# Kernel optimization log

Hardware: AMD Instinct MI355X
Metric: run time of the kernel (lower is better)

Reference implementation:

```python
import jax, jax.numpy as jnp
import numpy as np

# Block(type='a'): dim=256, mlp_ratio=2, qk_dim=64, att_cr=0.5 (pdim=128), sr=2, inp_group=1
DIM, QK, PD, HID, SR = 256, 64, 128, 512, 2
EPS = 1e-5
SCALE = QK ** -0.5


def _conv(x, w, stride=1, pad=0, groups=1):
    return jax.lax.conv_general_dilated(
        x, w, (stride, stride), [(pad, pad), (pad, pad)],
        feature_group_count=groups,
        dimension_numbers=('NCHW', 'OIHW', 'NCHW'))


def _bn(x, s, b):
    # BatchNorm2d in inference/reparam form: per-channel affine
    return x * s[:, None, None] + b[:, None, None]


def setup_inputs() -> dict:
    key = jax.random.key(0)
    ks = jax.random.split(key, 16)
    B, H, W = 16, 64, 64
    x = jax.random.normal(ks[0], (B, DIM, H, W), jnp.float32)
    def w(k, shape):  # conv weights
        return jax.random.normal(k, shape, jnp.float32) * 0.02
    def sb(k, c):     # bn scale / bias
        k1, k2 = jax.random.split(k)
        return (1.0 + 0.1 * jax.random.normal(k1, (c,), jnp.float32),
                0.1 * jax.random.normal(k2, (c,), jnp.float32))
    s_in, b_in = sb(ks[2], 2 * QK + DIM)
    s_k, b_k = sb(ks[4], QK)
    s_v, b_v = sb(ks[6], PD)
    s_out, b_out = sb(ks[8], DIM)
    s1, b1 = sb(ks[10], HID)
    s2, b2 = sb(ks[12], DIM)
    return dict(
        x=x,
        gn_w=1.0 + 0.1 * jax.random.normal(ks[13], (DIM,), jnp.float32),
        gn_b=0.1 * jax.random.normal(ks[14], (DIM,), jnp.float32),
        w_in=w(ks[1], (2 * QK + DIM, DIM, 3, 3)), s_in=s_in, b_in=b_in,
        w_k=w(ks[3], (QK, 1, SR, SR)), s_k=s_k, b_k=b_k,
        w_v=w(ks[5], (PD, 1, SR, SR)), s_v=s_v, b_v=b_v,
        w_out=w(ks[7], (DIM, DIM, 1, 1)), s_out=s_out, b_out=b_out,
        w1=w(ks[9], (HID, DIM, 1, 1)), s1=s1, b1=b1,
        w2=w(ks[11], (DIM, HID, 1, 1)), s2=s2, b2=b2,
    )


def reference(x, gn_w, gn_b, w_in, s_in, b_in, w_k, s_k, b_k, w_v, s_v, b_v,
              w_out, s_out, b_out, w1, s1, b1, w2, s2, b2):
    B, _, H, W = x.shape
    # --- LRSHA branch ---
    # GroupNorm(1, dim): normalize over (C,H,W) per sample, per-channel affine
    mu = jnp.mean(x, axis=(1, 2, 3), keepdims=True)
    var = jnp.var(x, axis=(1, 2, 3), keepdims=True)
    xn = (x - mu) * jax.lax.rsqrt(var + EPS)
    xn = xn * gn_w[:, None, None] + gn_b[:, None, None]
    t = _bn(_conv(xn, w_in, stride=1, pad=1), s_in, b_in)  # [B, 2*QK+DIM, H, W]
    q, k, v, u = jnp.split(t, [QK, 2 * QK, 2 * QK + PD], axis=1)
    k = _bn(_conv(k, w_k, stride=SR, groups=QK), s_k, b_k)  # [B,QK,H/2,W/2]
    v = _bn(_conv(v, w_v, stride=SR, groups=PD), s_v, b_v)  # [B,PD,H/2,W/2]
    qf = q.reshape(B, QK, H * W)          # [B, QK, N]
    kf = k.reshape(B, QK, -1)             # [B, QK, M]
    vf = v.reshape(B, PD, -1)             # [B, PD, M]
    attn = jax.nn.softmax(jnp.einsum('bcn,bcm->bnm', qf, kf) * SCALE, axis=-1)
    a = jnp.einsum('bpm,bnm->bpn', vf, attn).reshape(B, PD, H, W)
    cat = jnp.concatenate([a, u], axis=1)  # [B, DIM, H, W]
    att_out = _bn(_conv(jax.nn.relu(cat), w_out), s_out, b_out)
    x1 = x + att_out  # residual
    # --- FFN branch (1x1 conv -> ReLU -> 1x1 conv) ---
    h = jax.nn.relu(_bn(_conv(x1, w1), s1, b1))
    ffn = _bn(_conv(h, w2), s2, b2)
    return x1 + ffn
```

## Files before the change

kernel.cpp:

```cpp
#include <hip/hip_runtime.h>
#include <hip/hip_bf16.h>

#define DIM 256
#define QK 64
#define PD 128
#define HID 512
#define NPX 4096
#define NB 16
#define SCALE 0.125f
#define GN_EPS 1e-5f

typedef short bf16x8 __attribute__((ext_vector_type(8)));
typedef float f32x4 __attribute__((ext_vector_type(4)));
#define MFMA16(a, b, c) __builtin_amdgcn_mfma_f32_16x16x32_bf16(a, b, c, 0, 0, 0)

__device__ __forceinline__ unsigned f2b(float f) {
    unsigned u = __float_as_uint(f);
    return (u + 0x7fffu + ((u >> 16) & 1u)) >> 16;
}
__device__ __forceinline__ float b2f(unsigned short s) {
    return __uint_as_float((unsigned)s << 16);
}

__global__ __launch_bounds__(256) void gn_part_kernel(const float* __restrict__ x, float* __restrict__ part) {
    int chunk = blockIdx.x, b = blockIdx.y;
    const float* xp = x + (size_t)b * (DIM * NPX) + (size_t)chunk * 16384;
    float s = 0.f, ss = 0.f;
    for (int i = threadIdx.x; i < 16384; i += 256) { float v = xp[i]; s += v; ss += v * v; }
    for (int off = 32; off > 0; off >>= 1) { s += __shfl_down(s, off); ss += __shfl_down(ss, off); }
    __shared__ float red[8];
    int w = threadIdx.x >> 6;
    if ((threadIdx.x & 63) == 0) { red[w * 2] = s; red[w * 2 + 1] = ss; }
    __syncthreads();
    if (threadIdx.x == 0) {
        float S = red[0] + red[2] + red[4] + red[6];
        float SS = red[1] + red[3] + red[5] + red[7];
        part[(b * 64 + chunk) * 2] = S;
        part[(b * 64 + chunk) * 2 + 1] = SS;
    }
}

__global__ __launch_bounds__(256) void gn_final_kernel(const float* __restrict__ part,
                                                       const float* __restrict__ gn_w, const float* __restrict__ gn_b,
                                                       float* __restrict__ Aarr, float* __restrict__ Barr) {
    int b = blockIdx.x;
    float s = 0.f, ss = 0.f;
    if (threadIdx.x < 64) {
        s = part[(b * 64 + threadIdx.x) * 2];
        ss = part[(b * 64 + threadIdx.x) * 2 + 1];
        for (int off = 32; off > 0; off >>= 1) { s += __shfl_down(s, off); ss += __shfl_down(ss, off); }
    }
    __shared__ float sh[2];
    if (threadIdx.x == 0) {
        const float invN = 1.f / (float)(DIM * NPX);
        float mu = s * invN;
        float var = ss * invN - mu * mu;
        sh[0] = mu; sh[1] = rsqrtf(var + GN_EPS);
    }
    __syncthreads();
    float mu = sh[0], rstd = sh[1];
    int c = threadIdx.x;
    float g = gn_w[c] * rstd;
    Aarr[b * 256 + c] = g;
    Barr[b * 256 + c] = gn_b[c] - mu * g;
}

__global__ __launch_bounds__(256) void xnb_kernel(const float* __restrict__ x,
                                                  const float* __restrict__ Aarr, const float* __restrict__ Barr,
                                                  unsigned short* __restrict__ xb) {
    int y = blockIdx.x, b = blockIdx.y;
    int tid = threadIdx.x;
    __shared__ unsigned short tile[64 * 264];
    const float* xr = x + ((size_t)b << 20) + (size_t)y * 64;
    const float* Ab = Aarr + b * 256;
    const float* Bb = Barr + b * 256;
    for (int it = 0; it < 64; it++) {
        int lin = it * 256 + tid;
        int c = lin >> 6, px = lin & 63;
        float v = fmaf(xr[((size_t)c << 12) + px], Ab[c], Bb[c]);
        tile[px * 264 + c] = (unsigned short)f2b(v);
    }
    __syncthreads();
    unsigned short* ob = xb + (((size_t)(b * 64 + y)) << 14);
    for (int it = 0; it < 8; it++) {
        int lin = it * 256 + tid;
        int px = lin >> 5, g = lin & 31;
        *(uint4*)&ob[px * 256 + g * 8] = *(const uint4*)&tile[px * 264 + g * 8];
    }
}

__global__ __launch_bounds__(256) void wcvt_kernel(const float* __restrict__ w_in, const float* __restrict__ w_out,
                                                   const float* __restrict__ w1, const float* __restrict__ w2,
                                                   unsigned short* __restrict__ wb2, unsigned short* __restrict__ wob,
                                                   unsigned short* __restrict__ w1b, unsigned short* __restrict__ w2b) {
    int idx = blockIdx.x * 256 + threadIdx.x;
    if (idx < 884736) {
        int ci = idx & 31;
        int oc = (idx >> 5) % 384;
        int tapck = idx / 12288;
        int ck = tapck / 9, tap = tapck % 9;
        wb2[idx] = (unsigned short)f2b(w_in[((size_t)oc * 256 + ck * 32 + ci) * 9 + tap]);
    } else if (idx < 950272) {
        int j = idx - 884736;
        wob[j] = (unsigned short)f2b(w_out[j]);
    } else if (idx < 1081344) {
        int j = idx - 950272;
        w1b[j] = (unsigned short)f2b(w1[j]);
    } else if (idx < 1212416) {
        int j = idx - 1081344;
        w2b[j] = (unsigned short)f2b(w2[j]);
    }
}

__global__ __launch_bounds__(256, 3) void conv3_mfma_kernel(const unsigned short* __restrict__ xb,
                                                            const unsigned short* __restrict__ wb2,
                                                            const float* __restrict__ s_in, const float* __restrict__ b_in,
                                                            unsigned short* __restrict__ tcl) {
    int wgid = blockIdx.x;
    int tile = (wgid & 7) * 96 + (wgid >> 3);
    int ocb = tile % 6;
    int tmp = tile / 6;
    int rg2 = tmp & 7, b = tmp >> 3;
    int tid = threadIdx.x;
    int w = tid >> 6, lane = tid & 63, g = lane >> 4, l15 = lane & 15;
    __shared__ unsigned short xs[6 * 66 * 40];
    int oc0 = ocb * 64;
    if (tid < 48) {
        int row = tid >> 3, cp = (tid >> 2) & 1, gg = tid & 3;
        int col = cp ? 65 : 0;
        *(uint4*)&xs[(row * 66 + col) * 40 + gg * 8] = make_uint4(0, 0, 0, 0);
    }
    const unsigned short* xg = xb + ((size_t)b << 20);
    for (int half = 0; half < 2; half++) {
        int y0 = rg2 * 8 + half * 4;
        f32x4 acc[4][4];
#pragma unroll
        for (int o = 0; o < 4; o++)
#pragma unroll
            for (int p = 0; p < 4; p++)
#pragma unroll
                for (int r = 0; r < 4; r++) acc[o][p][r] = 0.f;
        for (int ck = 0; ck < 8; ck++) {
            int ci0 = ck * 32;
            __syncthreads();
#pragma unroll
            for (int it = 0; it < 6; it++) {
                int lin = it * 256 + tid;
                int gg = lin & 3, col = (lin >> 2) & 63, row = lin >> 8;
                int y = y0 - 1 + row;
                uint4 val = make_uint4(0, 0, 0, 0);
                if (y >= 0 && y < 64)
                    val = *(const uint4*)(xg + (((size_t)(y * 64 + col)) << 8) + ci0 + gg * 8);
                *(uint4*)&xs[(row * 66 + col + 1) * 40 + gg * 8] = val;
            }
            __syncthreads();
            const unsigned short* wp = wb2 + (size_t)ck * 9 * 384 * 32;
#pragma unroll
            for (int tap = 0; tap < 9; tap++) {
                int dy = tap / 3, dx = tap % 3;
                bf16x8 Af[4], Bf[4];
#pragma unroll
                for (int o = 0; o < 4; o++)
                    Af[o] = *(const bf16x8*)(wp + ((size_t)tap * 384 + oc0 + o * 16 + l15) * 32 + g * 8);
#pragma unroll
                for (int p = 0; p < 4; p++)
                    Bf[p] = *(const bf16x8*)&xs[((w + dy) * 66 + p * 16 + l15 + dx) * 40 + g * 8];
#pragma unroll
                for (int o = 0; o < 4; o++)
#pragma unroll
                    for (int p = 0; p < 4; p++)
                        acc[o][p] = MFMA16(Af[o], Bf[p], acc[o][p]);
            }
        }
        int y = y0 + w;
        unsigned short* tout = tcl + ((size_t)(b * 4096 + y * 64)) * 384;
#pragma unroll
        for (int o = 0; o < 4; o++) {
            int ocb4 = oc0 + o * 16 + 4 * g;
            float s0 = s_in[ocb4], s1 = s_in[ocb4 + 1], s2 = s_in[ocb4 + 2], s3 = s_in[ocb4 + 3];
            float b0 = b_in[ocb4], b1 = b_in[ocb4 + 1], b2 = b_in[ocb4 + 2], b3 = b_in[ocb4 + 3];
#pragma unroll
            for (int p = 0; p < 4; p++) {
                ushort4 h;
                h.x = (unsigned short)f2b(fmaf(acc[o][p][0], s0, b0));
                h.y = (unsigned short)f2b(fmaf(acc[o][p][1], s1, b1));
                h.z = (unsigned short)f2b(fmaf(acc[o][p][2], s2, b2));
                h.w = (unsigned short)f2b(fmaf(acc[o][p][3], s3, b3));
                *(ushort4*)&tout[(size_t)(p * 16 + l15) * 384 + ocb4] = h;
            }
        }
    }
}

__global__ __launch_bounds__(256) void dw_kernel(const unsigned short* __restrict__ tcl,
                                                 const float* __restrict__ w_k, const float* __restrict__ s_k, const float* __restrict__ b_k,
                                                 const float* __restrict__ w_v, const float* __restrict__ s_v, const float* __restrict__ b_v,
                                                 unsigned short* __restrict__ kd_t, unsigned short* __restrict__ vd_b) {
    int mg = blockIdx.x, b = blockIdx.y;
    int m0 = mg * 64;
    int tid = threadIdx.x;
    __shared__ unsigned short vt[128 * 68];
    {
        int c = tid & 63;
        float4 wk4 = *(const float4*)(w_k + c * 4);
        float sc = s_k[c], bi = b_k[c];
#pragma unroll 4
        for (int it = 0; it < 16; it++) {
            int ml = it * 4 + (tid >> 6);
            int m = m0 + ml, yo = m >> 5, xo = m & 31;
            const unsigned short* s = tcl + ((size_t)(b * 4096 + yo * 128 + xo * 2)) * 384 + 64 + c;
            float v = wk4.x * b2f(s[0]) + wk4.y * b2f(s[384]) + wk4.z * b2f(s[24576]) + wk4.w * b2f(s[24960]);
            kd_t[((size_t)(b * 1024 + m) << 6) + c] = (unsigned short)f2b(fmaf(v, sc, bi));
        }
    }
    {
        int c2 = tid & 127;
        float4 wv4 = *(const float4*)(w_v + c2 * 4);
        float sc = s_v[c2], bi = b_v[c2];
#pragma unroll 4
        for (int it = 0; it < 32; it++) {
            int ml = it * 2 + (tid >> 7);
            int m = m0 + ml, yo = m >> 5, xo = m & 31;
            const unsigned short* s = tcl + ((size_t)(b * 4096 + yo * 128 + xo * 2)) * 384 + 128 + c2;
            float v = wv4.x * b2f(s[0]) + wv4.y * b2f(s[384]) + wv4.z * b2f(s[24576]) + wv4.w * b2f(s[24960]);
            vt[c2 * 68 + ml] = (unsigned short)f2b(fmaf(v, sc, bi));
        }
    }
    __syncthreads();
    {
        int c2 = tid >> 1, part = tid & 1;
        unsigned short* dst = vd_b + (((size_t)(b * 128 + c2)) << 10) + m0 + part * 32;
        const unsigned short* src = &vt[c2 * 68 + part * 32];
#pragma unroll
        for (int j = 0; j < 8; j++)
            *(ushort4*)(dst + j * 4) = *(const ushort4*)(src + j * 4);
    }
}

__global__ __launch_bounds__(256) void attn_mfma_kernel(const unsigned short* __restrict__ tcl,
                                                        const unsigned short* __restrict__ kd_t,
                                                        const unsigned short* __restrict__ vd_b,
                                                        float* __restrict__ a_out) {
    int tid = threadIdx.x;
    int wid = tid >> 6, lane = tid & 63;
    int g = lane >> 4, l15 = lane & 15;
    int b = blockIdx.y;
    int n0 = (blockIdx.x * 4 + wid) * 32;

    __shared__ char KsB[8192];
    __shared__ char VsB[16384];

    bf16x8 qf[2][2];
#pragma unroll
    for (int nf = 0; nf < 2; nf++)
#pragma unroll
        for (int kc = 0; kc < 2; kc++)
            qf[nf][kc] = *(const bf16x8*)(tcl + ((size_t)(b * 4096 + n0 + 16 * nf + l15)) * 384 + kc * 32 + g * 8);

    f32x4 O[8][2];
#pragma unroll
    for (int pt = 0; pt < 8; pt++)
#pragma unroll
        for (int nf = 0; nf < 2; nf++)
#pragma unroll
            for (int r = 0; r < 4; r++) O[pt][nf][r] = 0.f;
    float mr[2] = {-1e30f, -1e30f}, lr[2] = {0.f, 0.f};

    const unsigned short* kb = kd_t + ((size_t)b << 16);
    const unsigned short* vb = vd_b + ((size_t)(b * 128) << 10);

    union BU { unsigned u[4]; bf16x8 v; };
    int srcA = l15 + ((g & 1) << 5);
    int srcB = srcA + 16;
    bool hi = (g >> 1) != 0;
    int srow = tid >> 3, sch = tid & 7;

    for (int mt = 0; mt < 16; mt++) {
        int m0 = mt * 64;
        __syncthreads();
#pragma unroll
        for (int it = 0; it < 2; it++) {
            int row = it * 32 + srow;
            uint4 v = *(const uint4*)(kb + (((size_t)(m0 + row)) << 6) + sch * 8);
            *(uint4*)(KsB + row * 128 + ((sch * 16) ^ ((row & 7) << 4))) = v;
        }
#pragma unroll
        for (int it = 0; it < 4; it++) {
            int row = it * 32 + srow;
            uint4 v = *(const uint4*)(vb + (((size_t)row) << 10) + m0 + sch * 8);
            *(uint4*)(VsB + row * 128 + ((sch * 16) ^ ((row & 7) << 4))) = v;
        }
        __syncthreads();
        f32x4 sp[4][2];
#pragma unroll
        for (int f = 0; f < 4; f++)
#pragma unroll
            for (int nf = 0; nf < 2; nf++)
#pragma unroll
                for (int r = 0; r < 4; r++) sp[f][nf][r] = 0.f;
#pragma unroll
        for (int f = 0; f < 4; f++) {
#pragma unroll
            for (int kc = 0; kc < 2; kc++) {
                bf16x8 kf = *(const bf16x8*)(KsB + (16 * f + l15) * 128 + ((kc * 64 + g * 16) ^ ((l15 & 7) << 4)));
                sp[f][0] = MFMA16(kf, qf[0][kc], sp[f][0]);
                sp[f][1] = MFMA16(kf, qf[1][kc], sp[f][1]);
            }
        }
        BU Bp[2][2];
#pragma unroll
        for (int nf = 0; nf < 2; nf++) {
            float tmax = -1e30f;
#pragma unroll
            for (int f = 0; f < 4; f++)
#pragma unroll
                for (int r = 0; r < 4; r++) tmax = fmaxf(tmax, sp[f][nf][r]);
            tmax = fmaxf(tmax, __shfl_xor(tmax, 16));
            tmax = fmaxf(tmax, __shfl_xor(tmax, 32));
            float newm = fmaxf(mr[nf], tmax * SCALE);
            float fac = __expf(mr[nf] - newm);
            float ps = 0.f;
            unsigned pl[4], ph[4];
#pragma unroll
            for (int f = 0; f < 4; f++) {
                float p0 = __expf(fmaf(sp[f][nf][0], SCALE, -newm));
                float p1 = __expf(fmaf(sp[f][nf][1], SCALE, -newm));
                float p2 = __expf(fmaf(sp[f][nf][2], SCALE, -newm));
                float p3 = __expf(fmaf(sp[f][nf][3], SCALE, -newm));
                ps += (p0 + p1) + (p2 + p3);
                pl[f] = f2b(p0) | (f2b(p1) << 16);
                ph[f] = f2b(p2) | (f2b(p3) << 16);
            }
            ps += __shfl_xor(ps, 16);
            ps += __shfl_xor(ps, 32);
            lr[nf] = fmaf(lr[nf], fac, ps);
            mr[nf] = newm;
#pragma unroll
            for (int pt = 0; pt < 8; pt++)
#pragma unroll
                for (int r = 0; r < 4; r++) O[pt][nf][r] *= fac;
#pragma unroll
            for (int kc = 0; kc < 2; kc++) {
                unsigned a0 = (unsigned)__shfl((int)pl[2 * kc], srcA);
                unsigned a1 = (unsigned)__shfl((int)ph[2 * kc], srcA);
                unsigned b0 = (unsigned)__shfl((int)pl[2 * kc + 1], srcA);
                unsigned b1 = (unsigned)__shfl((int)ph[2 * kc + 1], srcA);
                unsigned a2 = (unsigned)__shfl((int)pl[2 * kc], srcB);
                unsigned a3 = (unsigned)__shfl((int)ph[2 * kc], srcB);
                unsigned b2 = (unsigned)__shfl((int)pl[2 * kc + 1], srcB);
                unsigned b3 = (unsigned)__shfl((int)ph[2 * kc + 1], srcB);
                Bp[nf][kc].u[0] = hi ? b0 : a0;
                Bp[nf][kc].u[1] = hi ? b1 : a1;
                Bp[nf][kc].u[2] = hi ? b2 : a2;
                Bp[nf][kc].u[3] = hi ? b3 : a3;
            }
        }
#pragma unroll
        for (int pt = 0; pt < 8; pt++) {
            int p = pt * 16 + l15;
#pragma unroll
            for (int kc = 0; kc < 2; kc++) {
                bf16x8 vf = *(const bf16x8*)(VsB + p * 128 + ((kc * 64 + g * 16) ^ ((p & 7) << 4)));
                O[pt][0] = MFMA16(vf, Bp[0][kc].v, O[pt][0]);
                O[pt][1] = MFMA16(vf, Bp[1][kc].v, O[pt][1]);
            }
        }
    }
    float inv0 = 1.f / lr[0], inv1 = 1.f / lr[1];
#pragma unroll
    for (int pt = 0; pt < 8; pt++) {
#pragma unroll
        for (int r = 0; r < 4; r++) {
            int prow = pt * 16 + 4 * g + r;
            size_t base = (((size_t)(b * 128 + prow)) << 12) + n0 + l15;
            a_out[base] = O[pt][0][r] * inv0;
            a_out[base + 16] = O[pt][1][r] * inv1;
        }
    }
}

__global__ __launch_bounds__(256) void acl_kernel(const float* __restrict__ a_in, const unsigned short* __restrict__ tcl,
                                                  unsigned short* __restrict__ aucl) {
    int ng = blockIdx.x, b = blockIdx.y;
    int tid = threadIdx.x;
    __shared__ unsigned short tile[64 * 132];
    int n0 = ng * 64;
    int nl = tid & 63, c4 = tid >> 6;
    for (int it = 0; it < 32; it++) {
        int ci = it * 4 + c4;
        float v = a_in[(((size_t)b * 128 + ci) << 12) + n0 + nl];
        tile[nl * 132 + ci] = (unsigned short)f2b(fmaxf(v, 0.f));
    }
    __syncthreads();
    for (int it = 0; it < 4; it++) {
        int lin = it * 256 + tid;
        int n = lin >> 4, cg = lin & 15;
        *(uint4*)&aucl[((size_t)(b * 4096 + n0 + n)) * 256 + cg * 8] = *(const uint4*)&tile[n * 132 + cg * 8];
    }
    for (int it = 0; it < 4; it++) {
        int lin = it * 256 + tid;
        int n = lin >> 4, cg = lin & 15;
        bf16x8 v = *(const bf16x8*)(tcl + ((size_t)(b * 4096 + n0 + n)) * 384 + 256 + cg * 8);
#pragma unroll
        for (int j = 0; j < 8; j++) {
            unsigned short s = (unsigned short)v[j];
            v[j] = (short)((s & 0x8000u) ? 0 : s);
        }
        *(bf16x8*)(aucl + ((size_t)(b * 4096 + n0 + n)) * 256 + 128 + cg * 8) = v;
    }
}

__global__ __launch_bounds__(256) void catconv_mfma_kernel(const unsigned short* __restrict__ aucl,
                                                           const unsigned short* __restrict__ wob,
                                                           const float* __restrict__ x,
                                                           const float* __restrict__ s_out, const float* __restrict__ b_out,
                                                           float* __restrict__ out, unsigned short* __restrict__ x1cl) {
    int tid = threadIdx.x;
    int w = tid >> 6, lane = tid & 63, g = lane >> 4, l15 = lane & 15;
    int b = blockIdx.z;
    int px0 = blockIdx.x * 256 + w * 64;
    int co0 = blockIdx.y * 64;
    f32x4 acc[4][4];
#pragma unroll
    for (int o = 0; o < 4; o++)
#pragma unroll
        for (int p = 0; p < 4; p++)
#pragma unroll
            for (int r = 0; r < 4; r++) acc[o][p][r] = 0.f;
    const unsigned short* ab = aucl + (((size_t)b * 4096) << 8);
    for (int kc = 0; kc < 8; kc++) {
        bf16x8 Af[4], Bf[4];
#pragma unroll
        for (int o = 0; o < 4; o++)
            Af[o] = *(const bf16x8*)(wob + (size_t)(co0 + o * 16 + l15) * 256 + kc * 32 + g * 8);
#pragma unroll
        for (int p = 0; p < 4; p++)
            Bf[p] = *(const bf16x8*)(ab + ((size_t)(px0 + p * 16 + l15) << 8) + kc * 32 + g * 8);
#pragma unroll
        for (int o = 0; o < 4; o++)
#pragma unroll
            for (int p = 0; p < 4; p++)
                acc[o][p] = MFMA16(Af[o], Bf[p], acc[o][p]);
    }
#pragma unroll
    for (int o = 0; o < 4; o++) {
        int co_b = co0 + o * 16 + 4 * g;
#pragma unroll
        for (int r = 0; r < 4; r++) {
            int co = co_b + r;
            float sc = s_out[co], bi = b_out[co];
            size_t base = (((size_t)b * 256 + co) << 12) + px0 + l15;
#pragma unroll
            for (int p = 0; p < 4; p++) {
                float res = x[base + p * 16] + fmaf(acc[o][p][r], sc, bi);
                out[base + p * 16] = res;
                acc[o][p][r] = res;
            }
        }
#pragma unroll
        for (int p = 0; p < 4; p++) {
            ushort4 h;
            h.x = (unsigned short)f2b(acc[o][p][0]);
            h.y = (unsigned short)f2b(acc[o][p][1]);
            h.z = (unsigned short)f2b(acc[o][p][2]);
            h.w = (unsigned short)f2b(acc[o][p][3]);
            *(ushort4*)&x1cl[((size_t)(b * 4096 + px0 + p * 16 + l15)) * 256 + co_b] = h;
        }
    }
}

__global__ __launch_bounds__(256) void ffn1_mfma_kernel(const unsigned short* __restrict__ x1cl,
                                                        const unsigned short* __restrict__ w1b,
                                                        const float* __restrict__ s1, const float* __restrict__ b1,
                                                        unsigned short* __restrict__ hcl) {
    int tid = threadIdx.x;
    int w = tid >> 6, lane = tid & 63, g = lane >> 4, l15 = lane & 15;
    int b = blockIdx.z;
    int px0 = blockIdx.x * 256 + w * 64;
    int hc0 = blockIdx.y * 64;
    f32x4 acc[4][4];
#pragma unroll
    for (int p = 0; p < 4; p++)
#pragma unroll
        for (int o = 0; o < 4; o++)
#pragma unroll
            for (int r = 0; r < 4; r++) acc[p][o][r] = 0.f;
    const unsigned short* xb = x1cl + (((size_t)b * 4096) << 8);
    for (int kc = 0; kc < 8; kc++) {
        bf16x8 Af[4], Bf[4];
#pragma unroll
        for (int p = 0; p < 4; p++)
            Af[p] = *(const bf16x8*)(xb + ((size_t)(px0 + p * 16 + l15) << 8) + kc * 32 + g * 8);
#pragma unroll
        for (int o = 0; o < 4; o++)
            Bf[o] = *(const bf16x8*)(w1b + (size_t)(hc0 + o * 16 + l15) * 256 + kc * 32 + g * 8);
#pragma unroll
        for (int p = 0; p < 4; p++)
#pragma unroll
            for (int o = 0; o < 4; o++)
                acc[p][o] = MFMA16(Af[p], Bf[o], acc[p][o]);
    }
    unsigned short* hb = hcl + (((size_t)b * 4096) << 9);
#pragma unroll
    for (int o = 0; o < 4; o++) {
        int hc = hc0 + o * 16 + l15;
        float sc = s1[hc], bi = b1[hc];
#pragma unroll
        for (int p = 0; p < 4; p++) {
#pragma unroll
            for (int r = 0; r < 4; r++) {
                int px = px0 + p * 16 + 4 * g + r;
                hb[((size_t)px << 9) + hc] = (unsigned short)f2b(fmaxf(fmaf(acc[p][o][r], sc, bi), 0.f));
            }
        }
    }
}

__global__ __launch_bounds__(256) void ffn2_mfma_kernel(const unsigned short* __restrict__ hcl,
                                                        const unsigned short* __restrict__ w2b,
                                                        const float* __restrict__ s2, const float* __restrict__ b2,
                                                        float* __restrict__ out) {
    int tid = threadIdx.x;
    int w = tid >> 6, lane = tid & 63, g = lane >> 4, l15 = lane & 15;
    int b = blockIdx.z;
    int px0 = blockIdx.x * 256 + w * 64;
    int co0 = blockIdx.y * 64;
    f32x4 acc[4][4];
#pragma unroll
    for (int o = 0; o < 4; o++)
#pragma unroll
        for (int p = 0; p < 4; p++)
#pragma unroll
            for (int r = 0; r < 4; r++) acc[o][p][r] = 0.f;
    const unsigned short* hb = hcl + (((size_t)b * 4096) << 9);
    for (int kc = 0; kc < 16; kc++) {
        bf16x8 Af[4], Bf[4];
#pragma unroll
        for (int o = 0; o < 4; o++)
            Af[o] = *(const bf16x8*)(w2b + (size_t)(co0 + o * 16 + l15) * 512 + kc * 32 + g * 8);
#pragma unroll
        for (int p = 0; p < 4; p++)
            Bf[p] = *(const bf16x8*)(hb + ((size_t)(px0 + p * 16 + l15) << 9) + kc * 32 + g * 8);
#pragma unroll
        for (int o = 0; o < 4; o++)
#pragma unroll
            for (int p = 0; p < 4; p++)
                acc[o][p] = MFMA16(Af[o], Bf[p], acc[o][p]);
    }
#pragma unroll
    for (int o = 0; o < 4; o++) {
#pragma unroll
        for (int r = 0; r < 4; r++) {
            int co = co0 + o * 16 + 4 * g + r;
            float sc = s2[co], bi = b2[co];
            size_t base = (((size_t)b * 256 + co) << 12) + px0 + l15;
#pragma unroll
            for (int p = 0; p < 4; p++)
                out[base + p * 16] = out[base + p * 16] + fmaf(acc[o][p][r], sc, bi);
        }
    }
}

extern "C" void kernel_launch(void* const* d_in, const int* in_sizes, int n_in,
                              void* d_out, int out_size, void* d_ws, size_t ws_size,
                              hipStream_t stream) {
    const float* x    = (const float*)d_in[0];
    const float* gn_w = (const float*)d_in[1];
    const float* gn_b = (const float*)d_in[2];
    const float* w_in = (const float*)d_in[3];
    const float* s_in = (const float*)d_in[4];
    const float* b_in = (const float*)d_in[5];
    const float* w_k  = (const float*)d_in[6];
    const float* s_k  = (const float*)d_in[7];
    const float* b_k  = (const float*)d_in[8];
    const float* w_v  = (const float*)d_in[9];
    const float* s_v  = (const float*)d_in[10];
    const float* b_v  = (const float*)d_in[11];
    const float* w_out= (const float*)d_in[12];
    const float* s_out= (const float*)d_in[13];
    const float* b_out= (const float*)d_in[14];
    const float* w1   = (const float*)d_in[15];
    const float* s1   = (const float*)d_in[16];
    const float* b1   = (const float*)d_in[17];
    const float* w2   = (const float*)d_in[18];
    const float* s2   = (const float*)d_in[19];
    const float* b2   = (const float*)d_in[20];
    float* out = (float*)d_out;
    float* ws = (float*)d_ws;

    float* part = ws;
    float* Aarr = ws + 2048;
    float* Barr = ws + 6144;
    unsigned short* tcl = (unsigned short*)(ws + 10240);
    float* a = ws + 12593152;
    unsigned short* xb   = (unsigned short*)a;
    unsigned short* x1cl = (unsigned short*)a;
    unsigned short* aucl = (unsigned short*)(ws + 20981760);
    unsigned short* hcl  = (unsigned short*)(ws + 20981760);
    unsigned short* kd_t = (unsigned short*)(ws + 37758976);
    unsigned short* vd_b = (unsigned short*)(ws + 38283264);
    unsigned short* wb2  = (unsigned short*)(ws + 39331840);
    unsigned short* wob  = (unsigned short*)(ws + 39774208);
    unsigned short* w1b  = (unsigned short*)(ws + 39806976);
    unsigned short* w2b  = (unsigned short*)(ws + 39872512);

    gn_part_kernel<<<dim3(64, 16), 256, 0, stream>>>(x, part);
    gn_final_kernel<<<16, 256, 0, stream>>>(part, gn_w, gn_b, Aarr, Barr);
    xnb_kernel<<<dim3(64, 16), 256, 0, stream>>>(x, Aarr, Barr, xb);
    wcvt_kernel<<<4736, 256, 0, stream>>>(w_in, w_out, w1, w2, wb2, wob, w1b, w2b);
    conv3_mfma_kernel<<<768, 256, 0, stream>>>(xb, wb2, s_in, b_in, tcl);
    dw_kernel<<<dim3(16, 16), 256, 0, stream>>>(tcl, w_k, s_k, b_k, w_v, s_v, b_v, kd_t, vd_b);
    attn_mfma_kernel<<<dim3(32, 16), 256, 0, stream>>>(tcl, kd_t, vd_b, a);
    acl_kernel<<<dim3(64, 16), 256, 0, stream>>>(a, tcl, aucl);
    catconv_mfma_kernel<<<dim3(16, 4, 16), 256, 0, stream>>>(aucl, wob, x, s_out, b_out, out, x1cl);
    ffn1_mfma_kernel<<<dim3(16, 8, 16), 256, 0, stream>>>(x1cl, w1b, s1, b1, hcl);
    ffn2_mfma_kernel<<<dim3(16, 4, 16), 256, 0, stream>>>(hcl, w2b, s2, b2, out);
}
```

Baseline: 545.7 us.

## Use direct global-to-LDS loads with XOR swizzle and 64-channel chunks in conv3

The 3x3 input conv now stages input tiles with global_load_lds (direct global-to-LDS DMA) rather than loading into registers and storing to LDS. The LDS layout becomes 128 bytes per pixel with an XOR swizzle on 16-byte groups to avoid bank conflicts, and each chunk covers 64 input channels, halving the number of barrier-separated load phases. Each tap now issues twice as many MFMAs per LDS stage. The costs are higher LDS usage (about 50KB per block), which may limit occupancy under launch_bounds(256,3), and more weight fragments held in registers.

Result: slower. 617.7 us (+13.2%).

```diff
diff --git a/kernel.cpp b/kernel.cpp
--- a/kernel.cpp
+++ b/kernel.cpp
@@ -20,6 +20,10 @@
 }
 __device__ __forceinline__ float b2f(unsigned short s) {
     return __uint_as_float((unsigned)s << 16);
+}
+__device__ __forceinline__ void gl_lds16(void* lds, const void* g) {
+    __builtin_amdgcn_global_load_lds((const __attribute__((address_space(1))) unsigned*)g,
+                                     (__attribute__((address_space(3))) unsigned*)lds, 16, 0, 0);
 }
 
 __global__ __launch_bounds__(256) void gn_part_kernel(const float* __restrict__ x, float* __restrict__ part) {
@@ -123,14 +127,18 @@
     int rg2 = tmp & 7, b = tmp >> 3;
     int tid = threadIdx.x;
     int w = tid >> 6, lane = tid & 63, g = lane >> 4, l15 = lane & 15;
-    __shared__ unsigned short xs[6 * 66 * 40];
+    __shared__ char xs[6 * 66 * 128];
     int oc0 = ocb * 64;
-    if (tid < 48) {
-        int row = tid >> 3, cp = (tid >> 2) & 1, gg = tid & 3;
-        int col = cp ? 65 : 0;
-        *(uint4*)&xs[(row * 66 + col) * 40 + gg * 8] = make_uint4(0, 0, 0, 0);
+    if (tid < 96) {
+        int row = tid >> 4, cp = (tid >> 3) & 1, sub = tid & 7;
+        int c = cp ? 65 : 0;
+        *(uint4*)&xs[(row * 66 + c) * 128 + sub * 16] = make_uint4(0, 0, 0, 0);
     }
     const unsigned short* xg = xb + ((size_t)b << 20);
+    int sgx = lane >> 3;
+    int ssub = lane & 7;
+    int sc7 = (1 + sgx) & 7;
+    int ssrc = ssub ^ sc7;
     for (int half = 0; half < 2; half++) {
         int y0 = rg2 * 8 + half * 4;
         f32x4 acc[4][4];
@@ -140,36 +148,51 @@
             for (int p = 0; p < 4; p++)
 #pragma unroll
                 for (int r = 0; r < 4; r++) acc[o][p][r] = 0.f;
-        for (int ck = 0; ck < 8; ck++) {
-            int ci0 = ck * 32;
+        for (int ck = 0; ck < 4; ck++) {
+            int ci0 = ck * 64;
             __syncthreads();
 #pragma unroll
-            for (int it = 0; it < 6; it++) {
-                int lin = it * 256 + tid;
-                int gg = lin & 3, col = (lin >> 2) & 63, row = lin >> 8;
+            for (int j = 0; j < 12; j++) {
+                int t = j * 4 + w;
+                int row = t >> 3, gx = t & 7;
                 int y = y0 - 1 + row;
-                uint4 val = make_uint4(0, 0, 0, 0);
-                if (y >= 0 && y < 64)
-                    val = *(const uint4*)(xg + (((size_t)(y * 64 + col)) << 8) + ci0 + gg * 8);
-                *(uint4*)&xs[(row * 66 + col + 1) * 40 + gg * 8] = val;
+                char* ldsb = &xs[(row * 66 + 1 + gx * 8) * 128];
+                if (y >= 0 && y < 64) {
+                    int px = gx * 8 + sgx;
+                    const unsigned short* gp = xg + (((size_t)(y * 64 + px)) << 8) + ci0 + ssrc * 8;
+                    gl_lds16(ldsb, gp);
+                } else {
+                    *(uint4*)(ldsb + lane * 16) = make_uint4(0, 0, 0, 0);
+                }
             }
             __syncthreads();
-            const unsigned short* wp = wb2 + (size_t)ck * 9 * 384 * 32;
+            const unsigned short* wpA = wb2 + (size_t)(ck * 2) * 9 * 384 * 32;
+            const unsigned short* wpB = wb2 + (size_t)(ck * 2 + 1) * 9 * 384 * 32;
 #pragma unroll
             for (int tap = 0; tap < 9; tap++) {
                 int dy = tap / 3, dx = tap % 3;
-                bf16x8 Af[4], Bf[4];
-#pragma unroll
-                for (int o = 0; o < 4; o++)
-                    Af[o] = *(const bf16x8*)(wp + ((size_t)tap * 384 + oc0 + o * 16 + l15) * 32 + g * 8);
-#pragma unroll
-                for (int p = 0; p < 4; p++)
-                    Bf[p] = *(const bf16x8*)&xs[((w + dy) * 66 + p * 16 + l15 + dx) * 40 + g * 8];
-#pragma unroll
-                for (int o = 0; o < 4; o++)
-#pragma unroll
-                    for (int p = 0; p < 4; p++)
-                        acc[o][p] = MFMA16(Af[o], Bf[p], acc[o][p]);
+                bf16x8 Af[2][4], Bf[2][4];
+#pragma unroll
+                for (int o = 0; o < 4; o++) {
+                    size_t woff = ((size_t)tap * 384 + oc0 + o * 16 + l15) * 32 + g * 8;
+                    Af[0][o] = *(const bf16x8*)(wpA + woff);
+                    Af[1][o] = *(const bf16x8*)(wpB + woff);
+                }
+#pragma unroll
+                for (int p = 0; p < 4; p++) {
+                    int c = p * 16 + l15 + dx;
+                    int base = ((w + dy) * 66 + c) * 128;
+                    int c7 = c & 7;
+                    Bf[0][p] = *(const bf16x8*)&xs[base + ((g ^ c7) << 4)];
+                    Bf[1][p] = *(const bf16x8*)&xs[base + (((4 + g) ^ c7) << 4)];
+                }
+#pragma unroll
+                for (int kc = 0; kc < 2; kc++)
+#pragma unroll
+                    for (int o = 0; o < 4; o++)
+#pragma unroll
+                        for (int p = 0; p < 4; p++)
+                            acc[o][p] = MFMA16(Af[kc][o], Bf[kc][p], acc[o][p]);
             }
         }
         int y = y0 + w;
```

## Fuse attention output layout conversion into attention and catconv kernels

Applied to the files above, without the earlier changes.

The attention kernel now applies ReLU, converts its output to bf16 and writes it pixel-major through a shared-memory transpose, instead of writing fp32 channel-major. The separate acl kernel goes away: catconv reads the attention part from the new buffer and the u part straight from tcl, applying ReLU on load by zeroing negative bf16 values. This removes one launch plus the fp32 write and read of the intermediate tensor. The cost is an extra 34KB of LDS in the attention kernel, which may lower occupancy, and strided 384-wide reads of u inside the GEMM.

Measured after the change: 516.2 us. 5.4% less time.

```diff
diff --git a/kernel.cpp b/kernel.cpp
--- a/kernel.cpp
+++ b/kernel.cpp
@@ -240,7 +240,7 @@
 __global__ __launch_bounds__(256) void attn_mfma_kernel(const unsigned short* __restrict__ tcl,
                                                         const unsigned short* __restrict__ kd_t,
                                                         const unsigned short* __restrict__ vd_b,
-                                                        float* __restrict__ a_out) {
+                                                        unsigned short* __restrict__ apx) {
     int tid = threadIdx.x;
     int wid = tid >> 6, lane = tid & 63;
     int g = lane >> 4, l15 = lane & 15;
@@ -249,6 +249,7 @@
 
     __shared__ char KsB[8192];
     __shared__ char VsB[16384];
+    __shared__ unsigned short ot[4][32][136];
 
     bf16x8 qf[2][2];
 #pragma unroll
@@ -372,45 +373,20 @@
 #pragma unroll
         for (int r = 0; r < 4; r++) {
             int prow = pt * 16 + 4 * g + r;
-            size_t base = (((size_t)(b * 128 + prow)) << 12) + n0 + l15;
-            a_out[base] = O[pt][0][r] * inv0;
-            a_out[base + 16] = O[pt][1][r] * inv1;
-        }
-    }
-}
-
-__global__ __launch_bounds__(256) void acl_kernel(const float* __restrict__ a_in, const unsigned short* __restrict__ tcl,
-                                                  unsigned short* __restrict__ aucl) {
-    int ng = blockIdx.x, b = blockIdx.y;
-    int tid = threadIdx.x;
-    __shared__ unsigned short tile[64 * 132];
-    int n0 = ng * 64;
-    int nl = tid & 63, c4 = tid >> 6;
-    for (int it = 0; it < 32; it++) {
-        int ci = it * 4 + c4;
-        float v = a_in[(((size_t)b * 128 + ci) << 12) + n0 + nl];
-        tile[nl * 132 + ci] = (unsigned short)f2b(fmaxf(v, 0.f));
-    }
-    __syncthreads();
-    for (int it = 0; it < 4; it++) {
-        int lin = it * 256 + tid;
-        int n = lin >> 4, cg = lin & 15;
-        *(uint4*)&aucl[((size_t)(b * 4096 + n0 + n)) * 256 + cg * 8] = *(const uint4*)&tile[n * 132 + cg * 8];
-    }
-    for (int it = 0; it < 4; it++) {
-        int lin = it * 256 + tid;
-        int n = lin >> 4, cg = lin & 15;
-        bf16x8 v = *(const bf16x8*)(tcl + ((size_t)(b * 4096 + n0 + n)) * 384 + 256 + cg * 8);
-#pragma unroll
-        for (int j = 0; j < 8; j++) {
-            unsigned short s = (unsigned short)v[j];
-            v[j] = (short)((s & 0x8000u) ? 0 : s);
-        }
-        *(bf16x8*)(aucl + ((size_t)(b * 4096 + n0 + n)) * 256 + 128 + cg * 8) = v;
-    }
-}
-
-__global__ __launch_bounds__(256) void catconv_mfma_kernel(const unsigned short* __restrict__ aucl,
+            ot[wid][l15][prow]      = (unsigned short)f2b(fmaxf(O[pt][0][r] * inv0, 0.f));
+            ot[wid][l15 + 16][prow] = (unsigned short)f2b(fmaxf(O[pt][1][r] * inv1, 0.f));
+        }
+    }
+#pragma unroll
+    for (int j = 0; j < 8; j++) {
+        int lin = j * 64 + lane;
+        int row = lin >> 4, cg = lin & 15;
+        *(uint4*)&apx[((size_t)(b * 4096 + n0 + row)) * 128 + cg * 8] = *(const uint4*)&ot[wid][row][cg * 8];
+    }
+}
+
+__global__ __launch_bounds__(256) void catconv_mfma_kernel(const unsigned short* __restrict__ apx,
+                                                           const unsigned short* __restrict__ tcl,
                                                            const unsigned short* __restrict__ wob,
                                                            const float* __restrict__ x,
                                                            const float* __restrict__ s_out, const float* __restrict__ b_out,
@@ -427,15 +403,29 @@
         for (int p = 0; p < 4; p++)
 #pragma unroll
             for (int r = 0; r < 4; r++) acc[o][p][r] = 0.f;
-    const unsigned short* ab = aucl + (((size_t)b * 4096) << 8);
+    const unsigned short* ab = apx + (((size_t)b * 4096) << 7);
+    const unsigned short* ub = tcl + ((size_t)b * 4096) * 384 + 256;
     for (int kc = 0; kc < 8; kc++) {
         bf16x8 Af[4], Bf[4];
 #pragma unroll
         for (int o = 0; o < 4; o++)
             Af[o] = *(const bf16x8*)(wob + (size_t)(co0 + o * 16 + l15) * 256 + kc * 32 + g * 8);
-#pragma unroll
-        for (int p = 0; p < 4; p++)
-            Bf[p] = *(const bf16x8*)(ab + ((size_t)(px0 + p * 16 + l15) << 8) + kc * 32 + g * 8);
+        if (kc < 4) {
+#pragma unroll
+            for (int p = 0; p < 4; p++)
+                Bf[p] = *(const bf16x8*)(ab + ((size_t)(px0 + p * 16 + l15) << 7) + kc * 32 + g * 8);
+        } else {
+#pragma unroll
+            for (int p = 0; p < 4; p++) {
+                bf16x8 v = *(const bf16x8*)(ub + (size_t)(px0 + p * 16 + l15) * 384 + (kc - 4) * 32 + g * 8);
+#pragma unroll
+                for (int j = 0; j < 8; j++) {
+                    unsigned short s = (unsigned short)v[j];
+                    v[j] = (short)((s & 0x8000u) ? 0 : s);
+                }
+                Bf[p] = v;
+            }
+        }
 #pragma unroll
         for (int o = 0; o < 4; o++)
 #pragma unroll
@@ -592,10 +582,9 @@
     float* Aarr = ws + 2048;
     float* Barr = ws + 6144;
     unsigned short* tcl = (unsigned short*)(ws + 10240);
-    float* a = ws + 12593152;
-    unsigned short* xb   = (unsigned short*)a;
-    unsigned short* x1cl = (unsigned short*)a;
-    unsigned short* aucl = (unsigned short*)(ws + 20981760);
+    unsigned short* xb   = (unsigned short*)(ws + 12593152);
+    unsigned short* x1cl = (unsigned short*)(ws + 12593152);
+    unsigned short* apx  = (unsigned short*)(ws + 20981760);
     unsigned short* hcl  = (unsigned short*)(ws + 20981760);
     unsigned short* kd_t = (unsigned short*)(ws + 37758976);
     unsigned short* vd_b = (unsigned short*)(ws + 38283264);
@@ -610,9 +599,8 @@
     wcvt_kernel<<<4736, 256, 0, stream>>>(w_in, w_out, w1, w2, wb2, wob, w1b, w2b);
     conv3_mfma_kernel<<<768, 256, 0, stream>>>(xb, wb2, s_in, b_in, tcl);
     dw_kernel<<<dim3(16, 16), 256, 0, stream>>>(tcl, w_k, s_k, b_k, w_v, s_v, b_v, kd_t, vd_b);
-    attn_mfma_kernel<<<dim3(32, 16), 256, 0, stream>>>(tcl, kd_t, vd_b, a);
-    acl_kernel<<<dim3(64, 16), 256, 0, stream>>>(a, tcl, aucl);
-    catconv_mfma_kernel<<<dim3(16, 4, 16), 256, 0, stream>>>(aucl, wob, x, s_out, b_out, out, x1cl);
+    attn_mfma_kernel<<<dim3(32, 16), 256, 0, stream>>>(tcl, kd_t, vd_b, apx);
+    catconv_mfma_kernel<<<dim3(16, 4, 16), 256, 0, stream>>>(apx, tcl, wob, x, s_out, b_out, out, x1cl);
     ffn1_mfma_kernel<<<dim3(16, 8, 16), 256, 0, stream>>>(x1cl, w1b, s1, b1, hcl);
     ffn2_mfma_kernel<<<dim3(16, 4, 16), 256, 0, stream>>>(hcl, w2b, s2, b2, out);
 }
```
